# Performance work log

Measured on AMD Instinct MI355X. Metric: run time of the kernel, lower is better.

Reference implementation:

```python
import jax, jax.numpy as jnp
import numpy as np

H = 512   # GRU hidden size
D = 300   # word embedding size
Z = 128   # conditioning dim


def _gru_cell(x, h, Wih, Whh, bih, bhh):
    # torch.nn.GRUCell semantics
    gi = x @ Wih.T + bih          # [B, 3H]
    gh = h @ Whh.T + bhh          # [B, 3H]
    ir, iz, inn = jnp.split(gi, 3, axis=-1)
    hr, hz, hn = jnp.split(gh, 3, axis=-1)
    r = jax.nn.sigmoid(ir + hr)
    z = jax.nn.sigmoid(iz + hz)
    n = jnp.tanh(inn + r * hn)
    return (1.0 - z) * n + z * h


def setup_inputs() -> dict:
    key = jax.random.key(0)
    ks = jax.random.split(key, 16)
    B, S = 1024, 64
    text = jax.random.normal(ks[0], (B, S, D), jnp.float32)
    text_lengths = jax.random.randint(ks[1], (B,), 1, S + 1)  # >=1 avoids div-by-zero
    s = 1.0 / np.sqrt(H)

    def u(k, shape):
        return jax.random.uniform(k, shape, jnp.float32, -s, s)

    return {
        "text": text,
        "text_lengths": text_lengths,
        "Wih_f": u(ks[2], (3 * H, D)), "Whh_f": u(ks[3], (3 * H, H)),
        "bih_f": u(ks[4], (3 * H,)),   "bhh_f": u(ks[5], (3 * H,)),
        "Wih_b": u(ks[6], (3 * H, D)), "Whh_b": u(ks[7], (3 * H, H)),
        "bih_b": u(ks[8], (3 * H,)),   "bhh_b": u(ks[9], (3 * H,)),
        "W_mu": u(ks[10], (Z, H)),  "b_mu": u(ks[11], (Z,)),
        "W_sig": u(ks[12], (Z, H)), "b_sig": u(ks[13], (Z,)),
        "eps": jax.random.normal(ks[14], (B, Z), jnp.float32),
    }


def reference(text, text_lengths, Wih_f, Whh_f, bih_f, bhh_f,
              Wih_b, Whh_b, bih_b, bhh_b, W_mu, b_mu, W_sig, b_sig, eps):
    B, S, _ = text.shape
    xs = jnp.transpose(text, (1, 0, 2))                       # [S, B, D]
    mask = (jnp.arange(S)[:, None] < text_lengths[None, :]).astype(text.dtype)  # [S, B]
    h0 = jnp.zeros((B, H), text.dtype)

    def fstep(h, inp):
        x, m = inp
        h = _gru_cell(x, h, Wih_f, Whh_f, bih_f, bhh_f)
        return h, h * m[:, None]

    _, hf = jax.lax.scan(fstep, h0, (xs, mask))               # [S, B, H]

    def bstep(h, inp):
        x, m = inp
        h = _gru_cell(x, h, Wih_b, Whh_b, bih_b, bhh_b)
        return h, h * m[:, None]

    # backward pass reads text[-i-1] and masks with the FORWARD-index mask (as in original)
    _, hb_seq = jax.lax.scan(bstep, h0, (xs[::-1], mask))     # [S, B, H]
    # original stores backward step i at index (-i) mod S:
    # out[j] = hb_seq[(S - j) % S]  ==  roll(reverse(hb_seq), 1)
    hb = jnp.roll(hb_seq[::-1], 1, axis=0)

    words = (hf + hb) * 0.5                                   # [S, B, H]
    avg = words.sum(0) / mask.sum(0)[:, None]                 # [B, H]

    lrelu = lambda v: jnp.where(v >= 0, v, 0.2 * v)
    mu = lrelu(avg @ W_mu.T + b_mu)                           # [B, Z]
    sigma = jnp.exp(lrelu(avg @ W_sig.T + b_sig))             # [B, Z]
    final = eps * sigma + mu                                  # reparameterized sample
    return (final, mu, sigma)
```

## Files before the change

### kernel.cpp

```cpp
#include <hip/hip_runtime.h>

#define B_ 1024
#define S_ 64
#define D_ 300
#define DP_ 320
#define H_ 512
#define G3_ 1536
#define Z_ 128
#define NC1 10
#define NC2 16
#define CSTR 64

typedef __bf16 bf16x8 __attribute__((ext_vector_type(8)));
typedef float f32x4 __attribute__((ext_vector_type(4)));

#define GLLD(g, l) __builtin_amdgcn_global_load_lds( \
    (const __attribute__((address_space(1))) void*)(g), \
    (__attribute__((address_space(3))) void*)(l), 16, 0, 0)
#define GLLD_SYS(g, l) __builtin_amdgcn_global_load_lds( \
    (const __attribute__((address_space(1))) void*)(g), \
    (__attribute__((address_space(3))) void*)(l), 16, 0, 17)

#define MFMA(a, b, c) __builtin_amdgcn_mfma_f32_16x16x32_bf16((a), (b), (c), 0, 0, 0)

__global__ __launch_bounds__(256) void prep_cnt(unsigned* __restrict__ cnt) {
    int i = blockIdx.x * 256 + threadIdx.x;
    cnt[i] = 0u;
}

__global__ __launch_bounds__(320) void prep_text(const float* __restrict__ text,
                                                 __bf16* __restrict__ Xbf) {
    int bs = blockIdx.x;
    int b = bs >> 6, s = bs & 63;
    int dp = threadIdx.x;
    float v = (dp < D_) ? text[(size_t)bs * D_ + dp] : 0.f;
    Xbf[((size_t)s * B_ + b) * DP_ + dp] = (__bf16)v;
}

__global__ __launch_bounds__(256) void prep_w(
    const float* __restrict__ Wih_f, const float* __restrict__ Whh_f,
    const float* __restrict__ Wih_b, const float* __restrict__ Whh_b,
    const float* __restrict__ W_mu, const float* __restrict__ W_sig,
    __bf16* __restrict__ Wk1, __bf16* __restrict__ Wk2, __bf16* __restrict__ Wcat) {
    const int n1 = 2 * G3_ * DP_;
    const int n2 = 2 * G3_ * H_;
    int i = blockIdx.x * 256 + threadIdx.x;
    if (i < n1) {
        int dir = i / (G3_ * DP_);
        int rem = i - dir * (G3_ * DP_);
        int r = rem / DP_;
        int k = rem - r * DP_;
        const float* W = dir ? Wih_b : Wih_f;
        Wk1[i] = (k < D_) ? (__bf16)W[(size_t)r * D_ + k] : (__bf16)0.f;
    } else if (i < n1 + n2) {
        int jj = i - n1;
        int dir = jj / (G3_ * H_);
        int rem = jj - dir * (G3_ * H_);
        int r = rem / H_;
        int k = rem - r * H_;
        const float* W = dir ? Whh_b : Whh_f;
        Wk2[jj] = (__bf16)W[(size_t)r * H_ + k];
    } else {
        int idx = i - n1 - n2;
        int z = idx >> 9, k = idx & 511;
        Wcat[idx] = (__bf16)(z < 128 ? W_mu[(size_t)z * H_ + k]
                                     : W_sig[(size_t)(z - 128) * H_ + k]);
    }
}

__global__ __launch_bounds__(256, 1) void gru_persist(
    const __bf16* __restrict__ Xbf, const __bf16* __restrict__ Wk1,
    const __bf16* __restrict__ Wk2,
    const float* __restrict__ bih_f, const float* __restrict__ bhh_f,
    const float* __restrict__ bih_b, const float* __restrict__ bhh_b,
    const int* __restrict__ lens,
    __bf16* __restrict__ Hb0, __bf16* __restrict__ Hb1,
    float* __restrict__ Ssum, unsigned* __restrict__ cnt)
{
    __shared__ __align__(16) __bf16 hbuf[NC2 * 2048];
    __shared__ __align__(16) __bf16 xbuf[2 * NC1 * 2048];

    const int bid = blockIdx.x;
    const int xcd = bid & 7, slot = bid >> 3;
    const int dir = xcd >> 2;
    const int mb  = (xcd & 3) * 4 + (slot >> 3);
    const int jb  = slot & 7;
    const int b0  = mb * 64;
    const int group = dir * 16 + mb;
    unsigned* const gcnt = cnt + group * CSTR;

    const int tid = threadIdx.x;
    const int wave = tid >> 6;
    const int lane = tid & 63;

    const int jcol = jb * 64 + wave * 16 + (lane & 15);
    const int kq8  = (lane >> 4) * 8;

    const int srow = tid >> 2;
    const int scol = ((tid & 3) ^ ((tid >> 3) & 3)) * 8;
    const size_t hrow = (size_t)(dir * B_ + b0 + srow) * H_ + scol;

    {
        const int sx0 = dir ? (S_ - 1) : 0;
        const __bf16* src = Xbf + ((size_t)sx0 * B_ + b0 + srow) * DP_ + scol;
        __bf16* dst = xbuf + wave * 512;
#pragma unroll
        for (int c = 0; c < NC1; ++c)
            GLLD(src + c * 32, dst + c * 2048);
    }

    bf16x8 w1c[NC1][3];
    bf16x8 w2c[NC2][3];
    {
        const __bf16* w1p[3];
        const __bf16* w2p[3];
#pragma unroll
        for (int g = 0; g < 3; ++g) {
            w1p[g] = Wk1 + ((size_t)dir * G3_ + g * H_ + jcol) * DP_ + kq8;
            w2p[g] = Wk2 + ((size_t)dir * G3_ + g * H_ + jcol) * H_ + kq8;
        }
#pragma unroll
        for (int c = 0; c < NC1; ++c)
#pragma unroll
            for (int g = 0; g < 3; ++g)
                w1c[c][g] = *(const bf16x8*)(w1p[g] + c * 32);
#pragma unroll
        for (int c = 0; c < NC2; ++c)
#pragma unroll
            for (int g = 0; g < 3; ++g)
                w2c[c][g] = *(const bf16x8*)(w2p[g] + c * 32);
    }

    const float* bih = dir ? bih_b : bih_f;
    const float* bhh = dir ? bhh_b : bhh_f;
    const float b_r  = bih[jcol] + bhh[jcol];
    const float b_z  = bih[H_ + jcol] + bhh[H_ + jcol];
    const float b_ni = bih[2 * H_ + jcol];
    const float b_nh = bhh[2 * H_ + jcol];

    unsigned lenp[4];
#pragma unroll
    for (int mt = 0; mt < 4; ++mt) {
        int r0 = b0 + mt * 16 + (lane >> 4) * 4;
        lenp[mt] = (unsigned)(lens[r0] & 255) | ((unsigned)(lens[r0 + 1] & 255) << 8)
                 | ((unsigned)(lens[r0 + 2] & 255) << 16) | ((unsigned)(lens[r0 + 3] & 255) << 24);
    }

    float hreg[16], ssum[16];
#pragma unroll
    for (int i = 0; i < 16; ++i) { hreg[i] = 0.f; ssum[i] = 0.f; }

    const int qsl  = (lane >> 4) ^ ((lane >> 1) & 3);
    const int aoff = (lane & 15) * 32 + qsl * 8;

#define LDX(P, c) do { _Pragma("unroll") \
    for (int mt_ = 0; mt_ < 4; ++mt_) \
        P[mt_] = *(const bf16x8*)(xb + (c) * 2048 + aoff + mt_ * 512); } while (0)
#define LDH(P, c) do { _Pragma("unroll") \
    for (int mt_ = 0; mt_ < 4; ++mt_) \
        P[mt_] = *(const bf16x8*)(hbuf + (c) * 2048 + aoff + mt_ * 512); } while (0)
#define FMA1(P, c) do { _Pragma("unroll") \
    for (int mt_ = 0; mt_ < 4; ++mt_) { \
        acc[mt_][0] = MFMA(P[mt_], w1c[c][0], acc[mt_][0]); \
        acc[mt_][1] = MFMA(P[mt_], w1c[c][1], acc[mt_][1]); \
        acc[mt_][2] = MFMA(P[mt_], w1c[c][2], acc[mt_][2]); } } while (0)
#define FMA2(P, c) do { _Pragma("unroll") \
    for (int mt_ = 0; mt_ < 4; ++mt_) { \
        acc[mt_][0] = MFMA(P[mt_], w2c[c][0], acc[mt_][0]); \
        acc[mt_][1] = MFMA(P[mt_], w2c[c][1], acc[mt_][1]); \
        acc[mt_][3] = MFMA(P[mt_], w2c[c][2], acc[mt_][3]); } } while (0)

    __syncthreads();

    for (int s = 0; s < S_; ++s) {
        if (s < S_ - 1) {
            const int sxn = dir ? (S_ - 2 - s) : (s + 1);
            const __bf16* src = Xbf + ((size_t)sxn * B_ + b0 + srow) * DP_ + scol;
            __bf16* dst = xbuf + ((s + 1) & 1) * (NC1 * 2048) + wave * 512;
#pragma unroll
            for (int c = 0; c < NC1; ++c)
                GLLD(src + c * 32, dst + c * 2048);
        }

        f32x4 acc[4][4];
#pragma unroll
        for (int mt = 0; mt < 4; ++mt)
#pragma unroll
            for (int p = 0; p < 4; ++p)
                acc[mt][p] = (f32x4){0.f, 0.f, 0.f, 0.f};

        const __bf16* xb = xbuf + (s & 1) * (NC1 * 2048);
        bf16x8 pa[4], pb[4];

        LDX(pa, 0); LDX(pb, 1);
        FMA1(pa, 0); LDX(pa, 2);
        FMA1(pb, 1); LDX(pb, 3);
        FMA1(pa, 2); LDX(pa, 4);
        FMA1(pb, 3); LDX(pb, 5);

        if (s > 0) {
            if (tid == 0) {
                const unsigned tgt = 8u * (unsigned)s;
                unsigned it = 0;
                while (__hip_atomic_load(gcnt, __ATOMIC_RELAXED,
                                         __HIP_MEMORY_SCOPE_AGENT) < tgt) {
                    if (++it > (1u << 20)) break;
                }
            }
            __syncthreads();

            {
                const __bf16* src = (s & 1 ? Hb1 : Hb0) + hrow;
                __bf16* dst = hbuf + wave * 512;
#pragma unroll
                for (int c = 0; c < NC2; ++c)
                    GLLD_SYS(src + c * 32, dst + c * 2048);
            }
        }

        FMA1(pa, 4); LDX(pa, 6);
        FMA1(pb, 5); LDX(pb, 7);
        FMA1(pa, 6); LDX(pa, 8);
        FMA1(pb, 7); LDX(pb, 9);
        FMA1(pa, 8);
        FMA1(pb, 9);

        if (s > 0) {
            __syncthreads();

            LDH(pa, 0); LDH(pb, 1);
#pragma unroll
            for (int cc = 0; cc < 7; ++cc) {
                FMA2(pa, 2 * cc);     LDH(pa, 2 * cc + 2);
                FMA2(pb, 2 * cc + 1); LDH(pb, 2 * cc + 3);
            }
            FMA2(pa, 14);
            FMA2(pb, 15);
        }

        {
            __bf16* hb_w = (s & 1) ? Hb0 : Hb1;
            const bool store_lane = (lane & 1) == 0;
#pragma unroll
            for (int mt = 0; mt < 4; ++mt) {
#pragma unroll
                for (int reg = 0; reg < 4; ++reg) {
                    const int i = mt * 4 + reg;
                    const float r = 1.f / (1.f + __expf(-(acc[mt][0][reg] + b_r)));
                    const float z = 1.f / (1.f + __expf(-(acc[mt][1][reg] + b_z)));
                    const float nv = acc[mt][2][reg] + b_ni + r * (acc[mt][3][reg] + b_nh);
                    const float n = 2.f / (1.f + __expf(-2.f * nv)) - 1.f;
                    const float hnew = (1.f - z) * n + z * hreg[i];
                    hreg[i] = hnew;
                    if (((lenp[mt] >> (reg * 8)) & 255u) > (unsigned)s) ssum[i] += hnew;
                    __bf16 hb16 = (__bf16)hnew;
                    unsigned short myb = __builtin_bit_cast(unsigned short, hb16);
                    unsigned ob = (unsigned)__shfl_xor((int)(unsigned)myb, 1, 64);
                    if (store_lane) {
                        const int b = b0 + mt * 16 + (lane >> 4) * 4 + reg;
                        __hip_atomic_store(
                            (unsigned*)(hb_w + (size_t)(dir * B_ + b) * H_ + jcol),
                            (unsigned)myb | (ob << 16),
                            __ATOMIC_RELAXED, __HIP_MEMORY_SCOPE_AGENT);
                    }
                }
            }
        }
        __syncthreads();
        if (tid == 0 && s < S_ - 1)
            __hip_atomic_fetch_add(gcnt, 1u, __ATOMIC_RELAXED,
                                   __HIP_MEMORY_SCOPE_AGENT);
    }

#undef LDX
#undef LDH
#undef FMA1
#undef FMA2

#pragma unroll
    for (int mt = 0; mt < 4; ++mt)
#pragma unroll
        for (int reg = 0; reg < 4; ++reg) {
            const int b = b0 + mt * 16 + (lane >> 4) * 4 + reg;
            Ssum[(size_t)(dir * B_ + b) * H_ + jcol] = ssum[mt * 4 + reg];
        }
}

__global__ __launch_bounds__(128) void avg_prep(const float* __restrict__ Ssum,
                                                const int* __restrict__ lens,
                                                __bf16* __restrict__ Avg) {
    int b = blockIdx.x, t = threadIdx.x;
    float inv = 0.5f / (float)lens[b];
    float4 a = *(const float4*)(Ssum + (size_t)b * H_ + t * 4);
    float4 c = *(const float4*)(Ssum + (size_t)(B_ + b) * H_ + t * 4);
    __bf16* dst = Avg + (size_t)b * H_ + t * 4;
    dst[0] = (__bf16)((a.x + c.x) * inv);
    dst[1] = (__bf16)((a.y + c.y) * inv);
    dst[2] = (__bf16)((a.z + c.z) * inv);
    dst[3] = (__bf16)((a.w + c.w) * inv);
}

__global__ __launch_bounds__(256) void head_gemm(
    const __bf16* __restrict__ Avg, const __bf16* __restrict__ Wcat,
    const float* __restrict__ b_mu, const float* __restrict__ b_sig,
    float* __restrict__ out)
{
    __shared__ __align__(16) __bf16 abuf[16 * 2048];
    const int bid = blockIdx.x;
    const int mb = bid >> 2, jb = bid & 3;
    const int tid = threadIdx.x, wave = tid >> 6, lane = tid & 63;
    const int srow = tid >> 2, scol = (tid & 3) * 8;
    const __bf16* asrc = Avg + (size_t)(mb * 64 + srow) * H_ + scol;
    {
        __bf16* dst = abuf + wave * 512;
#pragma unroll
        for (int c = 0; c < 16; ++c) GLLD(asrc + c * 32, dst + c * 2048);
    }
    __syncthreads();
    const int j = jb * 64 + wave * 16 + (lane & 15);
    const int kq8 = (lane >> 4) * 8;
    const __bf16* wp = Wcat + (size_t)j * H_ + kq8;
    const int aoff = (lane & 15) * 32 + kq8;
    f32x4 acc[4];
#pragma unroll
    for (int mt = 0; mt < 4; ++mt) acc[mt] = (f32x4){0.f, 0.f, 0.f, 0.f};
#pragma unroll
    for (int c = 0; c < 16; ++c) {
        bf16x8 wf = *(const bf16x8*)(wp + c * 32);
#pragma unroll
        for (int mt = 0; mt < 4; ++mt) {
            bf16x8 af = *(const bf16x8*)(abuf + c * 2048 + aoff + mt * 512);
            acc[mt] = MFMA(af, wf, acc[mt]);
        }
    }
    const int gate = j >> 7, z = j & 127;
    const float bias = gate ? b_sig[z] : b_mu[z];
#pragma unroll
    for (int mt = 0; mt < 4; ++mt)
#pragma unroll
        for (int reg = 0; reg < 4; ++reg) {
            const int b = mb * 64 + mt * 16 + (lane >> 4) * 4 + reg;
            float v = acc[mt][reg] + bias;
            v = v >= 0.f ? v : 0.2f * v;
            if (gate) v = __expf(v);
            out[(size_t)(1 + gate) * B_ * Z_ + (size_t)b * Z_ + z] = v;
        }
}

__global__ __launch_bounds__(256) void final_k(const float* __restrict__ eps,
                                               float* __restrict__ out) {
    int i = blockIdx.x * 256 + threadIdx.x;
    out[i] = eps[i] * out[2 * B_ * Z_ + i] + out[B_ * Z_ + i];
}

extern "C" void kernel_launch(void* const* d_in, const int* in_sizes, int n_in,
                              void* d_out, int out_size, void* d_ws, size_t ws_size,
                              hipStream_t stream) {
    const float* text  = (const float*)d_in[0];
    const int*   lens  = (const int*)  d_in[1];
    const float* Wih_f = (const float*)d_in[2];
    const float* Whh_f = (const float*)d_in[3];
    const float* bih_f = (const float*)d_in[4];
    const float* bhh_f = (const float*)d_in[5];
    const float* Wih_b = (const float*)d_in[6];
    const float* Whh_b = (const float*)d_in[7];
    const float* bih_b = (const float*)d_in[8];
    const float* bhh_b = (const float*)d_in[9];
    const float* W_mu  = (const float*)d_in[10];
    const float* b_mu  = (const float*)d_in[11];
    const float* W_sig = (const float*)d_in[12];
    const float* b_sig = (const float*)d_in[13];
    const float* eps   = (const float*)d_in[14];
    float* out = (float*)d_out;

    char* ws = (char*)d_ws;
    __bf16* Xbf  = (__bf16*)(ws);
    __bf16* Wk1  = (__bf16*)(ws + 41943040);
    __bf16* Wk2  = (__bf16*)(ws + 43909120);
    __bf16* Hb0  = (__bf16*)(ws + 47054848);
    __bf16* Hb1  = (__bf16*)(ws + 49152000);
    float*  Ssum = (float*) (ws + 51249152);
    __bf16* Avg  = (__bf16*)(ws + 55443456);
    __bf16* Wcat = (__bf16*)(ws + 56492032);
    unsigned* cntp = (unsigned*)(ws + 56754176);

    prep_cnt<<<8, 256, 0, stream>>>(cntp);
    prep_text<<<B_ * S_, 320, 0, stream>>>(text, Xbf);
    prep_w<<<10496, 256, 0, stream>>>(Wih_f, Whh_f, Wih_b, Whh_b, W_mu, W_sig,
                                      Wk1, Wk2, Wcat);

    void* args[] = { (void*)&Xbf, (void*)&Wk1, (void*)&Wk2,
                     (void*)&bih_f, (void*)&bhh_f, (void*)&bih_b, (void*)&bhh_b,
                     (void*)&lens, (void*)&Hb0, (void*)&Hb1,
                     (void*)&Ssum, (void*)&cntp };
    hipError_t ce = hipLaunchCooperativeKernel((void*)gru_persist, dim3(256),
                                               dim3(256), args, 0, stream);
    if (ce != hipSuccess) {
        gru_persist<<<256, 256, 0, stream>>>(Xbf, Wk1, Wk2,
                                             bih_f, bhh_f, bih_b, bhh_b,
                                             lens, Hb0, Hb1, Ssum, cntp);
    }

    avg_prep<<<B_, 128, 0, stream>>>(Ssum, lens, Avg);
    head_gemm<<<64, 256, 0, stream>>>(Avg, Wcat, b_mu, b_sig, out);
    final_k<<<512, 256, 0, stream>>>(eps, out);
}
```

Baseline: 938.2 us.

## Replace group counter barrier with per-producer flags and chunked pipelined h consumption

Each of the 8 column blocks in a group now publishes its own step flag instead of all blocks bumping one shared atomic counter. Consumers poll the flags in pairs and start the DMA for each producer's slice of h as soon as that slice is ready. The recurrent MFMA work then runs in four chunks, each gated by a vmcnt wait and a barrier, so compute overlaps the arrival of later slices. This removes the serialized global wait and the full syncthreads before any h load, at the cost of every thread spinning on flags, hand-written waitcnt ordering, and a much smaller spin timeout.

After: 1.116 ms. +19.0%, slower.

```diff
diff --git a/kernel.cpp b/kernel.cpp
--- a/kernel.cpp
+++ b/kernel.cpp
@@ -22,6 +22,10 @@
     (__attribute__((address_space(3))) void*)(l), 16, 0, 17)
 
 #define MFMA(a, b, c) __builtin_amdgcn_mfma_f32_16x16x32_bf16((a), (b), (c), 0, 0, 0)
+
+#define WAITV(N) asm volatile("s_waitcnt vmcnt(" #N ")" ::: "memory")
+#define SBAR() __builtin_amdgcn_s_barrier()
+#define SFENCE() __builtin_amdgcn_sched_barrier(0)
 
 __global__ __launch_bounds__(256) void prep_cnt(unsigned* __restrict__ cnt) {
     int i = blockIdx.x * 256 + threadIdx.x;
@@ -87,7 +91,7 @@
     const int jb  = slot & 7;
     const int b0  = mb * 64;
     const int group = dir * 16 + mb;
-    unsigned* const gcnt = cnt + group * CSTR;
+    unsigned* const gflag = cnt + group * CSTR;
 
     const int tid = threadIdx.x;
     const int wave = tid >> 6;
@@ -169,6 +173,21 @@
         acc[mt_][0] = MFMA(P[mt_], w2c[c][0], acc[mt_][0]); \
         acc[mt_][1] = MFMA(P[mt_], w2c[c][1], acc[mt_][1]); \
         acc[mt_][3] = MFMA(P[mt_], w2c[c][2], acc[mt_][3]); } } while (0)
+#define POLL2(p0, p1) do { unsigned it_ = 0; \
+    while (__hip_atomic_load(gflag + (p0) * 8, __ATOMIC_RELAXED, \
+                             __HIP_MEMORY_SCOPE_AGENT) < (unsigned)s || \
+           __hip_atomic_load(gflag + (p1) * 8, __ATOMIC_RELAXED, \
+                             __HIP_MEMORY_SCOPE_AGENT) < (unsigned)s) { \
+        if (++it_ > (1u << 16)) break; } } while (0)
+#define HDMA(p) do { \
+    GLLD_SYS(hsrc + (p) * 64,      hbuf + (p) * 4096 + wave * 512); \
+    GLLD_SYS(hsrc + (p) * 64 + 32, hbuf + (p) * 4096 + 2048 + wave * 512); } while (0)
+#define CONSUME4(c0) do { \
+    LDH(pa, c0); LDH(pb, (c0) + 1); \
+    FMA2(pa, c0); LDH(pa, (c0) + 2); \
+    FMA2(pb, (c0) + 1); LDH(pb, (c0) + 3); \
+    FMA2(pa, (c0) + 2); \
+    FMA2(pb, (c0) + 3); } while (0)
 
     __syncthreads();
 
@@ -190,34 +209,20 @@
                 acc[mt][p] = (f32x4){0.f, 0.f, 0.f, 0.f};
 
         const __bf16* xb = xbuf + (s & 1) * (NC1 * 2048);
+        const __bf16* hsrc = ((s & 1) ? Hb1 : Hb0) + hrow;
         bf16x8 pa[4], pb[4];
 
         LDX(pa, 0); LDX(pb, 1);
         FMA1(pa, 0); LDX(pa, 2);
         FMA1(pb, 1); LDX(pb, 3);
+
+        if (s > 0) {
+            POLL2(0, 1); HDMA(0); HDMA(1);
+            POLL2(2, 3); HDMA(2); HDMA(3);
+        }
+
         FMA1(pa, 2); LDX(pa, 4);
         FMA1(pb, 3); LDX(pb, 5);
-
-        if (s > 0) {
-            if (tid == 0) {
-                const unsigned tgt = 8u * (unsigned)s;
-                unsigned it = 0;
-                while (__hip_atomic_load(gcnt, __ATOMIC_RELAXED,
-                                         __HIP_MEMORY_SCOPE_AGENT) < tgt) {
-                    if (++it > (1u << 20)) break;
-                }
-            }
-            __syncthreads();
-
-            {
-                const __bf16* src = (s & 1 ? Hb1 : Hb0) + hrow;
-                __bf16* dst = hbuf + wave * 512;
-#pragma unroll
-                for (int c = 0; c < NC2; ++c)
-                    GLLD_SYS(src + c * 32, dst + c * 2048);
-            }
-        }
-
         FMA1(pa, 4); LDX(pa, 6);
         FMA1(pb, 5); LDX(pb, 7);
         FMA1(pa, 6); LDX(pa, 8);
@@ -226,16 +231,20 @@
         FMA1(pb, 9);
 
         if (s > 0) {
-            __syncthreads();
-
-            LDH(pa, 0); LDH(pb, 1);
-#pragma unroll
-            for (int cc = 0; cc < 7; ++cc) {
-                FMA2(pa, 2 * cc);     LDH(pa, 2 * cc + 2);
-                FMA2(pb, 2 * cc + 1); LDH(pb, 2 * cc + 3);
-            }
-            FMA2(pa, 14);
-            FMA2(pb, 15);
+            POLL2(4, 5); HDMA(4); HDMA(5);
+            WAITV(8);
+            SBAR(); SFENCE();
+            CONSUME4(0);
+            POLL2(6, 7); HDMA(6); HDMA(7);
+            WAITV(8);
+            SBAR(); SFENCE();
+            CONSUME4(4);
+            WAITV(4);
+            SBAR(); SFENCE();
+            CONSUME4(8);
+            WAITV(0);
+            SBAR(); SFENCE();
+            CONSUME4(12);
         }
 
         {
@@ -268,14 +277,17 @@
         }
         __syncthreads();
         if (tid == 0 && s < S_ - 1)
-            __hip_atomic_fetch_add(gcnt, 1u, __ATOMIC_RELAXED,
-                                   __HIP_MEMORY_SCOPE_AGENT);
+            __hip_atomic_store(gflag + jb * 8, (unsigned)(s + 1),
+                               __ATOMIC_RELAXED, __HIP_MEMORY_SCOPE_AGENT);
     }
 
 #undef LDX
 #undef LDH
 #undef FMA1
 #undef FMA2
+#undef POLL2
+#undef HDMA
+#undef CONSUME4
 
 #pragma unroll
     for (int mt = 0; mt < 4; ++mt)
```
